# Kernel tuning notes

Measured on AMD Instinct MI355X. Metric: run time of the kernel, lower is better.

The kernel has to match this reference:

```python
import jax, jax.numpy as jnp
import numpy as np

N_ENT, N_REL, RANK = 40943, 11, 256
IMG_DIM, LING_DIM = 1000, 768
BATCH = 1000
ALPHA, GAMMA, SCALE = 0.1, 0.8, 100.0
REG, SINKHORN_ITERS, NUM_OT = 0.05, 100, 10


def _sinkhorn_plan(mm_row, st_row):
    """Entropic-OT plan between uniform marginals over mm_dim and st_dim.
    Cost (as in cal_ot): ((st[:,None]-mm[None,:])**2 * scale).T -> [mm_dim, st_dim].
    Log-domain Sinkhorn for stability. Returns plan of shape [mm_dim, st_dim]."""
    mm_dim, st_dim = mm_row.shape[0], st_row.shape[0]
    M = ((st_row[:, None] - mm_row[None, :]) ** 2 * SCALE).T  # [mm_dim, st_dim]
    logK = -M / REG
    loga = -jnp.log(jnp.float32(mm_dim))  # uniform marginal log-prob
    logb = -jnp.log(jnp.float32(st_dim))
    f0 = jnp.zeros((mm_dim,), M.dtype)
    g0 = jnp.zeros((st_dim,), M.dtype)

    def body(i, fg):
        f, g = fg
        f = REG * (loga - jax.nn.logsumexp(logK + g[None, :] / REG, axis=1))
        g = REG * (logb - jax.nn.logsumexp(logK + f[:, None] / REG, axis=0))
        return (f, g)

    f, g = jax.lax.fori_loop(0, SINKHORN_ITERS, body, (f0, g0))
    return jnp.exp(logK + (f[:, None] + g[None, :]) / REG)


def _cal_ot(mm_vec, st_emb, delta_ot):
    # torch code runs this under no_grad -> stop_gradient on the OT part.
    plans = jax.vmap(_sinkhorn_plan)(mm_vec[:NUM_OT], st_emb[:NUM_OT])  # [10, mm_dim, st_dim]
    st_dim = st_emb.shape[-1]
    return jax.lax.stop_gradient(plans.mean(axis=0) * st_dim * SCALE) + delta_ot


def setup_inputs() -> dict:
    key = jax.random.key(0)
    ks = jax.random.split(key, 9)
    heads = jax.random.randint(ks[0], (BATCH,), 0, N_ENT)
    rels = jax.random.randint(ks[1], (BATCH,), 0, N_REL)
    tails = jax.random.randint(ks[2], (BATCH,), 0, N_ENT)
    x = jnp.stack([heads, rels, tails], axis=1).astype(jnp.int64)
    emb_ent = jax.random.normal(ks[3], (N_ENT, 2 * RANK), jnp.float32) * 0.001
    emb_rel = jax.random.normal(ks[4], (N_REL, 2 * RANK), jnp.float32) * 0.001
    xav_img = float(np.sqrt(2.0 / (IMG_DIM + 2 * RANK)))
    xav_ling = float(np.sqrt(2.0 / (LING_DIM + 2 * RANK)))
    mats_img = jax.random.normal(ks[5], (IMG_DIM, 2 * RANK), jnp.float32) * xav_img
    mats_ling = jax.random.normal(ks[6], (LING_DIM, 2 * RANK), jnp.float32) * xav_ling
    img_vec = jax.random.normal(ks[7], (N_ENT, IMG_DIM), jnp.float32)
    ling_vec = jax.random.normal(ks[8], (N_ENT, LING_DIM), jnp.float32)
    return {"x": x, "emb_ent": emb_ent, "emb_rel": emb_rel, "mats_img": mats_img,
            "mats_ling": mats_ling, "img_vec": img_vec, "ling_vec": ling_vec}


def reference(x, emb_ent, emb_rel, mats_img, mats_ling, img_vec, ling_vec):
    matrix1 = _cal_ot(img_vec, emb_ent, mats_img)    # [img_dim, 2r]
    matrix2 = _cal_ot(ling_vec, emb_ent, mats_ling)  # [ling_dim, 2r]
    img_embeddings = img_vec @ matrix1               # [n_ent, 2r]
    ling_embeddings = ling_vec @ matrix2             # [n_ent, 2r]
    embedding = (1.0 - ALPHA - GAMMA) * emb_ent + ALPHA * img_embeddings + GAMMA * ling_embeddings

    lhs = embedding[x[:, 0]]  # [B, 2r]
    rel = emb_rel[x[:, 1]]
    rhs = embedding[x[:, 2]]
    l0, l1 = lhs[:, :RANK], lhs[:, RANK:]
    r0, r1 = rel[:, :RANK], rel[:, RANK:]
    h0, h1 = rhs[:, :RANK], rhs[:, RANK:]
    t0, t1 = embedding[:, :RANK], embedding[:, RANK:]

    scores = (l0 * r0 - l1 * r1) @ t0.T + (l0 * r1 + l1 * r0) @ t1.T  # [B, n_ent]
    factors = (jnp.sqrt(l0 ** 2 + l1 ** 2),
               jnp.sqrt(r0 ** 2 + r1 ** 2),
               jnp.sqrt(h0 ** 2 + h1 ** 2))
    return scores, factors
```

## Files before the change

kernel.cpp:

```cpp
#include <hip/hip_runtime.h>

#define NENT 40943

typedef short bf16x8 __attribute__((ext_vector_type(8)));
typedef float f32x4 __attribute__((ext_vector_type(4)));

__device__ __forceinline__ unsigned short f2bf(float f) {
  unsigned int u = __builtin_bit_cast(unsigned int, f);
  u += 0x7fffu + ((u >> 16) & 1u);
  return (unsigned short)(u >> 16);
}
__device__ __forceinline__ float bf2f(unsigned short h) {
  unsigned int u = ((unsigned int)h) << 16;
  return __builtin_bit_cast(float, u);
}

#define K2C 2885.3900817779268f

__device__ __forceinline__ float aload(const float* p) {
  return __hip_atomic_load(p, __ATOMIC_RELAXED, __HIP_MEMORY_SCOPE_AGENT);
}
__device__ __forceinline__ void astore(float* p, float v) {
  __hip_atomic_store(p, v, __ATOMIC_RELAXED, __HIP_MEMORY_SCOPE_AGENT);
}

__global__ void init_k(const float* __restrict__ emb_ent, const float* __restrict__ img,
                       const float* __restrict__ ling, float* __restrict__ phi,
                       float* __restrict__ gam, float* __restrict__ A2, float* __restrict__ B2,
                       float* __restrict__ C2, unsigned int* __restrict__ flags) {
  const int p = blockIdx.x, t = threadIdx.x;
  const int pm = p % 10;
  const bool isImg = (p < 10);
  const int D = isImg ? 1000 : 768;
  const float* st = emb_ent + (size_t)pm * 512;
  const float* mm = isImg ? (img + (size_t)pm * 1000) : (ling + (size_t)pm * 768);
  for (int s = t; s < 512; s += 256) {
    float sv = st[s];
    A2[p * 512 + s] = -K2C * sv * sv;
    B2[p * 512 + s] = 2.f * K2C * sv;
    gam[p * 512 + s] = 0.f;
  }
  for (int m = t; m < 1024; m += 256) {
    float c2 = 0.f;
    if (m < D) { float mv = mm[m]; c2 = -K2C * mv * mv; }
    C2[p * 1024 + m] = c2;
    phi[p * 1024 + m] = 0.f;
  }
  if (t < 12) flags[p * 192 + t * 16] = 0u;
}

__global__ __launch_bounds__(512) void sinkhorn_k(
    const float* __restrict__ img, const float* __restrict__ ling,
    float* __restrict__ phi, float* __restrict__ gam,
    const float* __restrict__ A2, const float* __restrict__ B2,
    const float* __restrict__ C2, unsigned int* __restrict__ flags) {
  const int bid = blockIdx.x;
  const int p = bid / 12, j = bid % 12;
  const int pm = p % 10;
  const bool isImg = (p < 10);
  const int D = isImg ? 1000 : 768;
  const float* mm = isImg ? (img + (size_t)pm * 1000) : (ling + (size_t)pm * 768);
  float* phiP = phi + p * 1024;
  float* gamP = gam + p * 512;
  const float* A2P = A2 + p * 512;
  const float* B2P = B2 + p * 512;
  const float* C2P = C2 + p * 1024;
  unsigned int* flagP = flags + p * 192;
  const float negLog2D = isImg ? -9.965784284662087f : -9.584962500721156f;

  const int TPMF = isImg ? 6 : 8;
  const int fChunk = isImg ? 84 : 64;
  const int fm0 = j * fChunk;
  int fCount = D - fm0; if (fCount > fChunk) fCount = fChunk;
  const int gs0 = j * 43;
  int gCount = 512 - gs0; if (gCount > 43) gCount = 43;

  __shared__ float2 wb[512];
  __shared__ float2 um[1024];
  __shared__ float redM[512];
  __shared__ float redA[512];

  const int t = threadIdx.x;
  if (t < 512) wb[t].y = B2P[t];
  for (int m = t; m < D; m += 512) um[m].y = mm[m];

  const int fml = t / TPMF, fq = t - fml * TPMF;
  const bool fAct = (fml < fCount);
  const int fs0 = (fq * 512) / TPMF, fs1 = ((fq + 1) * 512) / TPMF;
  const int fmG = fm0 + fml;
  float fmm = 0.f, fC2 = 0.f;
  if (fAct) { fmm = mm[fmG]; fC2 = C2P[fmG]; }

  const int TPMG = 11;
  const int gsl = t / TPMG, gq = t - gsl * TPMG;
  const bool gAct = (gsl < gCount);
  const int gm0 = (gq * D) / TPMG, gm1 = ((gq + 1) * D) / TPMG;
  const int gsG = gs0 + gsl;
  float gA2 = 0.f;
  if (gAct) gA2 = A2P[gsG];

  unsigned int phase = 0;

  for (int it = 0; it < 100; ++it) {
    if (t < 512) wb[t].x = A2P[t] + aload(&gamP[t]);
    __syncthreads();
    if (fAct) {
      float vmax = -3.0e38f;
      for (int s = fs0; s < fs1; ++s) {
        float2 w = wb[s];
        vmax = fmaxf(vmax, fmaf(w.y, fmm, w.x));
      }
      float acc = 0.f;
      for (int s = fs0; s < fs1; ++s) {
        float2 w = wb[s];
        acc += __builtin_exp2f(fmaf(w.y, fmm, w.x) - vmax);
      }
      redM[t] = vmax; redA[t] = acc;
    }
    __syncthreads();
    if (fAct && fq == 0) {
      float vmax = redM[t], acc = redA[t];
      for (int q = 1; q < TPMF; ++q) {
        float m2 = redM[t + q], a2 = redA[t + q];
        float M = fmaxf(vmax, m2);
        acc = acc * __builtin_exp2f(vmax - M) + a2 * __builtin_exp2f(m2 - M);
        vmax = M;
      }
      astore(&phiP[fmG], negLog2D - fC2 - vmax - __builtin_log2f(acc));
    }
    phase++;
    __syncthreads();
    if (t == 0)
      __hip_atomic_store(flagP + j * 16, phase, __ATOMIC_RELAXED, __HIP_MEMORY_SCOPE_AGENT);
    if (t < 12) {
      while (__hip_atomic_load(flagP + t * 16, __ATOMIC_RELAXED, __HIP_MEMORY_SCOPE_AGENT) < phase)
        __builtin_amdgcn_s_sleep(1);
    }
    __syncthreads();

    for (int m = t; m < D; m += 512) um[m].x = C2P[m] + aload(&phiP[m]);
    __syncthreads();
    if (gAct) {
      float bs = wb[gsG].y;
      float vmax = -3.0e38f;
      for (int m = gm0; m < gm1; ++m) {
        float2 u = um[m];
        vmax = fmaxf(vmax, fmaf(u.y, bs, u.x));
      }
      float acc = 0.f;
      for (int m = gm0; m < gm1; ++m) {
        float2 u = um[m];
        acc += __builtin_exp2f(fmaf(u.y, bs, u.x) - vmax);
      }
      redM[t] = vmax; redA[t] = acc;
    }
    __syncthreads();
    if (gAct && gq == 0) {
      float vmax = redM[t], acc = redA[t];
      for (int q = 1; q < TPMG; ++q) {
        float m2 = redM[t + q], a2 = redA[t + q];
        float M = fmaxf(vmax, m2);
        acc = acc * __builtin_exp2f(vmax - M) + a2 * __builtin_exp2f(m2 - M);
        vmax = M;
      }
      astore(&gamP[gsG], -9.0f - gA2 - vmax - __builtin_log2f(acc));
    }
    phase++;
    __syncthreads();
    if (t == 0)
      __hip_atomic_store(flagP + j * 16, phase, __ATOMIC_RELAXED, __HIP_MEMORY_SCOPE_AGENT);
    if (t < 12) {
      while (__hip_atomic_load(flagP + t * 16, __ATOMIC_RELAXED, __HIP_MEMORY_SCOPE_AGENT) < phase)
        __builtin_amdgcn_s_sleep(1);
    }
    __syncthreads();
  }
}

__global__ void build_b(const float* __restrict__ mats_img, const float* __restrict__ mats_ling,
                        const float* __restrict__ img, const float* __restrict__ ling,
                        const float* __restrict__ phi, const float* __restrict__ gam,
                        const float* __restrict__ A2, const float* __restrict__ B2,
                        const float* __restrict__ C2, unsigned short* __restrict__ BbigT) {
  const int k = blockIdx.x, t = threadIdx.x;
  if (k >= 1768) {
    for (int n = t; n < 512; n += 256) BbigT[(size_t)n * 1792 + k] = 0;
    return;
  }
  const bool isImg = (k < 1000);
  const int kk = isImg ? k : (k - 1000);
  __shared__ float sU[10], sMM[10];
  if (t < 10) {
    const int p = isImg ? t : (10 + t);
    sU[t] = C2[p * 1024 + kk] + phi[p * 1024 + kk];
    sMM[t] = isImg ? img[(size_t)t * 1000 + kk] : ling[(size_t)t * 768 + kk];
  }
  __syncthreads();
  const float* mats = isImg ? mats_img : mats_ling;
  const float scale = isImg ? 0.1f : 0.8f;
  const int pbase = isImg ? 0 : 10;
  for (int n = t; n < 512; n += 256) {
    float val = 0.f;
    #pragma unroll
    for (int i = 0; i < 10; ++i) {
      const int p = pbase + i;
      float a = A2[p * 512 + n] + gam[p * 512 + n];
      float b = B2[p * 512 + n];
      val += __builtin_exp2f(fmaf(b, sMM[i], a + sU[i]));
    }
    float outv = scale * fmaf(5120.f, val, mats[(size_t)kk * 512 + n]);
    BbigT[(size_t)n * 1792 + k] = f2bf(outv);
  }
}

__global__ __launch_bounds__(256) void gemm1_k(
    const float* __restrict__ img, const float* __restrict__ ling,
    const float* __restrict__ emb_ent, const unsigned short* __restrict__ BbigT,
    unsigned short* __restrict__ Eb) {
  const int bid0 = blockIdx.x;
  const int wg = (bid0 & 7) * 160 + (bid0 >> 3);
  const int nt = wg & 3, mt = wg >> 2;
  const int m0 = mt * 128, n0 = nt * 128;
  __shared__ __align__(16) unsigned short As[128 * 40];
  __shared__ __align__(16) unsigned short Bs[128 * 40];
  const int t = threadIdx.x;
  const int wave = t >> 6, lane = t & 63;
  const int quad = lane >> 4, lrow = lane & 15;
  const int wm = (wave & 1) * 64, wn = (wave >> 1) * 64;
  f32x4 acc[4][4];
  #pragma unroll
  for (int a = 0; a < 4; ++a)
    #pragma unroll
    for (int b = 0; b < 4; ++b) acc[a][b] = (f32x4){0.f, 0.f, 0.f, 0.f};

  const int r = t >> 1, h = t & 1;
  const int gm = m0 + r;
  const bool mOK = (gm < NENT);
  const float* arowI = img + (size_t)gm * 1000;
  const float* arowL = ling + (size_t)gm * 768;
  const unsigned short* brow = BbigT + (size_t)(n0 + r) * 1792;
  unsigned short* asDst = As + r * 40 + h * 16;
  unsigned short* bsDst = Bs + r * 40 + h * 16;

  for (int k0 = 0; k0 < 1792; k0 += 32) {
    const int ck = k0 + h * 16;
    unsigned short u[16];
    #pragma unroll
    for (int q4 = 0; q4 < 4; ++q4) {
      const int kk = ck + q4 * 4;
      f32x4 v = (f32x4){0.f, 0.f, 0.f, 0.f};
      if (mOK) {
        if (kk < 1000) v = *(const f32x4*)(arowI + kk);
        else if (kk < 1768) v = *(const f32x4*)(arowL + (kk - 1000));
      }
      u[q4 * 4 + 0] = f2bf(v.x); u[q4 * 4 + 1] = f2bf(v.y);
      u[q4 * 4 + 2] = f2bf(v.z); u[q4 * 4 + 3] = f2bf(v.w);
    }
    bf16x8 w0, w1;
    #pragma unroll
    for (int i2 = 0; i2 < 8; ++i2) { w0[i2] = (short)u[i2]; w1[i2] = (short)u[8 + i2]; }
    *(bf16x8*)asDst = w0;
    *(bf16x8*)(asDst + 8) = w1;
    bf16x8 b0 = *(const bf16x8*)(brow + ck);
    bf16x8 b1 = *(const bf16x8*)(brow + ck + 8);
    *(bf16x8*)bsDst = b0;
    *(bf16x8*)(bsDst + 8) = b1;
    __syncthreads();
    bf16x8 af[4], bfv[4];
    #pragma unroll
    for (int i2 = 0; i2 < 4; ++i2) {
      af[i2] = *(const bf16x8*)(As + (wm + i2 * 16 + lrow) * 40 + quad * 8);
      bfv[i2] = *(const bf16x8*)(Bs + (wn + i2 * 16 + lrow) * 40 + quad * 8);
    }
    #pragma unroll
    for (int mi = 0; mi < 4; ++mi)
      #pragma unroll
      for (int ni = 0; ni < 4; ++ni)
        acc[mi][ni] = __builtin_amdgcn_mfma_f32_16x16x32_bf16(af[mi], bfv[ni], acc[mi][ni], 0, 0, 0);
    __syncthreads();
  }
  #pragma unroll
  for (int mi = 0; mi < 4; ++mi) {
    const int mbase = m0 + wm + mi * 16 + quad * 4;
    #pragma unroll
    for (int ni = 0; ni < 4; ++ni) {
      const int n = n0 + wn + ni * 16 + lrow;
      #pragma unroll
      for (int rr = 0; rr < 4; ++rr) {
        const int gm2 = mbase + rr;
        if (gm2 < NENT) {
          float v = acc[mi][ni][rr] + 0.1f * emb_ent[(size_t)gm2 * 512 + n];
          Eb[(size_t)gm2 * 512 + n] = f2bf(v);
        }
      }
    }
  }
}

__global__ void gather_c(const int* __restrict__ x, const unsigned short* __restrict__ Eb,
                         const float* __restrict__ emb_rel, unsigned short* __restrict__ cb,
                         float* __restrict__ outF) {
  const int i = blockIdx.x, t = threadIdx.x;
  if (i >= 1000) {
    cb[(size_t)i * 512 + t] = 0;
    cb[(size_t)i * 512 + 256 + t] = 0;
    return;
  }
  const int hI = x[i * 3 + 0], rI = x[i * 3 + 1], tI = x[i * 3 + 2];
  const float l0 = bf2f(Eb[(size_t)hI * 512 + t]);
  const float l1 = bf2f(Eb[(size_t)hI * 512 + 256 + t]);
  const float r0 = emb_rel[(size_t)rI * 512 + t];
  const float r1 = emb_rel[(size_t)rI * 512 + 256 + t];
  const float h0 = bf2f(Eb[(size_t)tI * 512 + t]);
  const float h1 = bf2f(Eb[(size_t)tI * 512 + 256 + t]);
  cb[(size_t)i * 512 + t] = f2bf(l0 * r0 - l1 * r1);
  cb[(size_t)i * 512 + 256 + t] = f2bf(l0 * r1 + l1 * r0);
  outF[(size_t)i * 256 + t] = sqrtf(l0 * l0 + l1 * l1);
  outF[256000 + (size_t)i * 256 + t] = sqrtf(r0 * r0 + r1 * r1);
  outF[512000 + (size_t)i * 256 + t] = sqrtf(h0 * h0 + h1 * h1);
}

__global__ __launch_bounds__(256) void gemm2_k(
    const unsigned short* __restrict__ cb, const unsigned short* __restrict__ Eb,
    float* __restrict__ scores) {
  const int bid0 = blockIdx.x;
  const int wg = (bid0 & 7) * 320 + (bid0 >> 3);
  const int mt = wg & 7, nt = wg >> 3;
  const int m0 = mt * 128, n0 = nt * 128;
  __shared__ __align__(16) unsigned short As[128 * 40];
  __shared__ __align__(16) unsigned short Bs[128 * 40];
  const int t = threadIdx.x;
  const int wave = t >> 6, lane = t & 63;
  const int quad = lane >> 4, lrow = lane & 15;
  const int wm = (wave & 1) * 64, wn = (wave >> 1) * 64;
  f32x4 acc[4][4];
  #pragma unroll
  for (int a = 0; a < 4; ++a)
    #pragma unroll
    for (int b = 0; b < 4; ++b) acc[a][b] = (f32x4){0.f, 0.f, 0.f, 0.f};

  const int r = t >> 1, h = t & 1;
  const unsigned short* arow = cb + (size_t)(m0 + r) * 512;
  const int ge = n0 + r;
  const bool nOK = (ge < NENT);
  const unsigned short* browE = Eb + (size_t)ge * 512;
  unsigned short* asDst = As + r * 40 + h * 16;
  unsigned short* bsDst = Bs + r * 40 + h * 16;

  for (int k0 = 0; k0 < 512; k0 += 32) {
    const int ck = k0 + h * 16;
    bf16x8 a0 = *(const bf16x8*)(arow + ck);
    bf16x8 a1 = *(const bf16x8*)(arow + ck + 8);
    *(bf16x8*)asDst = a0;
    *(bf16x8*)(asDst + 8) = a1;
    bf16x8 b0 = (bf16x8)0, b1 = (bf16x8)0;
    if (nOK) { b0 = *(const bf16x8*)(browE + ck); b1 = *(const bf16x8*)(browE + ck + 8); }
    *(bf16x8*)bsDst = b0;
    *(bf16x8*)(bsDst + 8) = b1;
    __syncthreads();
    bf16x8 af[4], bfv[4];
    #pragma unroll
    for (int i2 = 0; i2 < 4; ++i2) {
      af[i2] = *(const bf16x8*)(As + (wm + i2 * 16 + lrow) * 40 + quad * 8);
      bfv[i2] = *(const bf16x8*)(Bs + (wn + i2 * 16 + lrow) * 40 + quad * 8);
    }
    #pragma unroll
    for (int mi = 0; mi < 4; ++mi)
      #pragma unroll
      for (int ni = 0; ni < 4; ++ni)
        acc[mi][ni] = __builtin_amdgcn_mfma_f32_16x16x32_bf16(af[mi], bfv[ni], acc[mi][ni], 0, 0, 0);
    __syncthreads();
  }
  #pragma unroll
  for (int mi = 0; mi < 4; ++mi) {
    const int mbase = m0 + wm + mi * 16 + quad * 4;
    #pragma unroll
    for (int ni = 0; ni < 4; ++ni) {
      const int n = n0 + wn + ni * 16 + lrow;
      if (n < NENT) {
        #pragma unroll
        for (int rr = 0; rr < 4; ++rr) {
          const int i = mbase + rr;
          if (i < 1000) scores[(size_t)i * NENT + n] = acc[mi][ni][rr];
        }
      }
    }
  }
}

extern "C" void kernel_launch(void* const* d_in, const int* in_sizes, int n_in,
                              void* d_out, int out_size, void* d_ws, size_t ws_size,
                              hipStream_t stream) {
  (void)in_sizes; (void)n_in; (void)out_size; (void)ws_size;
  const int*   x        = (const int*)d_in[0];
  const float* emb_ent  = (const float*)d_in[1];
  const float* emb_rel  = (const float*)d_in[2];
  const float* mats_img = (const float*)d_in[3];
  const float* mats_ling= (const float*)d_in[4];
  const float* img_vec  = (const float*)d_in[5];
  const float* ling_vec = (const float*)d_in[6];
  float* out = (float*)d_out;

  float* phi = (float*)d_ws;
  float* gam = phi + 20 * 1024;
  float* A2  = gam + 20 * 512;
  float* B2  = A2 + 20 * 512;
  float* C2  = B2 + 20 * 512;
  unsigned int* flags = (unsigned int*)(C2 + 20 * 1024);
  unsigned short* BbigT = (unsigned short*)(flags + 20 * 192);
  unsigned short* Eb = BbigT + (size_t)512 * 1792;
  unsigned short* cb = Eb + (size_t)NENT * 512;

  init_k<<<dim3(20), dim3(256), 0, stream>>>(emb_ent, img_vec, ling_vec, phi, gam, A2, B2, C2, flags);
  sinkhorn_k<<<dim3(240), dim3(512), 0, stream>>>(img_vec, ling_vec, phi, gam, A2, B2, C2, flags);
  build_b<<<dim3(1792), dim3(256), 0, stream>>>(mats_img, mats_ling, img_vec, ling_vec,
                                                phi, gam, A2, B2, C2, BbigT);
  gemm1_k<<<dim3(1280), dim3(256), 0, stream>>>(img_vec, ling_vec, emb_ent, BbigT, Eb);
  gather_c<<<dim3(1024), dim3(256), 0, stream>>>(x, Eb, emb_rel, cb, out + (size_t)1000 * NENT);
  gemm2_k<<<dim3(2560), dim3(256), 0, stream>>>(cb, Eb, out);
}
```

Baseline: 3.163 ms.

## Replace in-kernel grid barrier Sinkhorn loop with per-iteration kernel launches

After: 3.512 ms. 11.1% more time.

```diff
diff --git a/kernel.cpp b/kernel.cpp
--- a/kernel.cpp
+++ b/kernel.cpp
@@ -17,17 +17,10 @@
 
 #define K2C 2885.3900817779268f
 
-__device__ __forceinline__ float aload(const float* p) {
-  return __hip_atomic_load(p, __ATOMIC_RELAXED, __HIP_MEMORY_SCOPE_AGENT);
-}
-__device__ __forceinline__ void astore(float* p, float v) {
-  __hip_atomic_store(p, v, __ATOMIC_RELAXED, __HIP_MEMORY_SCOPE_AGENT);
-}
-
 __global__ void init_k(const float* __restrict__ emb_ent, const float* __restrict__ img,
                        const float* __restrict__ ling, float* __restrict__ phi,
                        float* __restrict__ gam, float* __restrict__ A2, float* __restrict__ B2,
-                       float* __restrict__ C2, unsigned int* __restrict__ flags) {
+                       float* __restrict__ C2) {
   const int p = blockIdx.x, t = threadIdx.x;
   const int pm = p % 10;
   const bool isImg = (p < 10);
@@ -46,14 +39,13 @@
     C2[p * 1024 + m] = c2;
     phi[p * 1024 + m] = 0.f;
   }
-  if (t < 12) flags[p * 192 + t * 16] = 0u;
-}
-
-__global__ __launch_bounds__(512) void sinkhorn_k(
+}
+
+__global__ __launch_bounds__(512) void sink_f(
     const float* __restrict__ img, const float* __restrict__ ling,
-    float* __restrict__ phi, float* __restrict__ gam,
+    float* __restrict__ phi, const float* __restrict__ gam,
     const float* __restrict__ A2, const float* __restrict__ B2,
-    const float* __restrict__ C2, unsigned int* __restrict__ flags) {
+    const float* __restrict__ C2) {
   const int bid = blockIdx.x;
   const int p = bid / 12, j = bid % 12;
   const int pm = p % 10;
@@ -61,28 +53,24 @@
   const int D = isImg ? 1000 : 768;
   const float* mm = isImg ? (img + (size_t)pm * 1000) : (ling + (size_t)pm * 768);
   float* phiP = phi + p * 1024;
-  float* gamP = gam + p * 512;
+  const float* gamP = gam + p * 512;
   const float* A2P = A2 + p * 512;
   const float* B2P = B2 + p * 512;
   const float* C2P = C2 + p * 1024;
-  unsigned int* flagP = flags + p * 192;
   const float negLog2D = isImg ? -9.965784284662087f : -9.584962500721156f;
 
   const int TPMF = isImg ? 6 : 8;
   const int fChunk = isImg ? 84 : 64;
   const int fm0 = j * fChunk;
   int fCount = D - fm0; if (fCount > fChunk) fCount = fChunk;
-  const int gs0 = j * 43;
-  int gCount = 512 - gs0; if (gCount > 43) gCount = 43;
 
   __shared__ float2 wb[512];
-  __shared__ float2 um[1024];
   __shared__ float redM[512];
   __shared__ float redA[512];
 
   const int t = threadIdx.x;
-  if (t < 512) wb[t].y = B2P[t];
-  for (int m = t; m < D; m += 512) um[m].y = mm[m];
+  wb[t].x = A2P[t] + gamP[t];
+  wb[t].y = B2P[t];
 
   const int fml = t / TPMF, fq = t - fml * TPMF;
   const bool fAct = (fml < fCount);
@@ -90,90 +78,96 @@
   const int fmG = fm0 + fml;
   float fmm = 0.f, fC2 = 0.f;
   if (fAct) { fmm = mm[fmG]; fC2 = C2P[fmG]; }
+  __syncthreads();
+
+  if (fAct) {
+    float vmax = -3.0e38f;
+    for (int s = fs0; s < fs1; ++s) {
+      float2 w = wb[s];
+      vmax = fmaxf(vmax, fmaf(w.y, fmm, w.x));
+    }
+    float acc = 0.f;
+    for (int s = fs0; s < fs1; ++s) {
+      float2 w = wb[s];
+      acc += __builtin_exp2f(fmaf(w.y, fmm, w.x) - vmax);
+    }
+    redM[t] = vmax; redA[t] = acc;
+  }
+  __syncthreads();
+  if (fAct && fq == 0) {
+    float vmax = redM[t], acc = redA[t];
+    for (int q = 1; q < TPMF; ++q) {
+      float m2 = redM[t + q], a2 = redA[t + q];
+      float M = fmaxf(vmax, m2);
+      acc = acc * __builtin_exp2f(vmax - M) + a2 * __builtin_exp2f(m2 - M);
+      vmax = M;
+    }
+    phiP[fmG] = negLog2D - fC2 - vmax - __builtin_log2f(acc);
+  }
+}
+
+__global__ __launch_bounds__(512) void sink_g(
+    const float* __restrict__ img, const float* __restrict__ ling,
+    const float* __restrict__ phi, float* __restrict__ gam,
+    const float* __restrict__ A2, const float* __restrict__ B2,
+    const float* __restrict__ C2) {
+  const int bid = blockIdx.x;
+  const int p = bid / 12, j = bid % 12;
+  const int pm = p % 10;
+  const bool isImg = (p < 10);
+  const int D = isImg ? 1000 : 768;
+  const float* mm = isImg ? (img + (size_t)pm * 1000) : (ling + (size_t)pm * 768);
+  const float* phiP = phi + p * 1024;
+  float* gamP = gam + p * 512;
+  const float* A2P = A2 + p * 512;
+  const float* B2P = B2 + p * 512;
+  const float* C2P = C2 + p * 1024;
+
+  const int gs0 = j * 43;
+  int gCount = 512 - gs0; if (gCount > 43) gCount = 43;
+
+  __shared__ float2 um[1024];
+  __shared__ float redM[512];
+  __shared__ float redA[512];
+
+  const int t = threadIdx.x;
+  for (int m = t; m < D; m += 512) {
+    um[m].x = C2P[m] + phiP[m];
+    um[m].y = mm[m];
+  }
 
   const int TPMG = 11;
   const int gsl = t / TPMG, gq = t - gsl * TPMG;
   const bool gAct = (gsl < gCount);
   const int gm0 = (gq * D) / TPMG, gm1 = ((gq + 1) * D) / TPMG;
   const int gsG = gs0 + gsl;
-  float gA2 = 0.f;
-  if (gAct) gA2 = A2P[gsG];
-
-  unsigned int phase = 0;
-
-  for (int it = 0; it < 100; ++it) {
-    if (t < 512) wb[t].x = A2P[t] + aload(&gamP[t]);
-    __syncthreads();
-    if (fAct) {
-      float vmax = -3.0e38f;
-      for (int s = fs0; s < fs1; ++s) {
-        float2 w = wb[s];
-        vmax = fmaxf(vmax, fmaf(w.y, fmm, w.x));
-      }
-      float acc = 0.f;
-      for (int s = fs0; s < fs1; ++s) {
-        float2 w = wb[s];
-        acc += __builtin_exp2f(fmaf(w.y, fmm, w.x) - vmax);
-      }
-      redM[t] = vmax; redA[t] = acc;
-    }
-    __syncthreads();
-    if (fAct && fq == 0) {
-      float vmax = redM[t], acc = redA[t];
-      for (int q = 1; q < TPMF; ++q) {
-        float m2 = redM[t + q], a2 = redA[t + q];
-        float M = fmaxf(vmax, m2);
-        acc = acc * __builtin_exp2f(vmax - M) + a2 * __builtin_exp2f(m2 - M);
-        vmax = M;
-      }
-      astore(&phiP[fmG], negLog2D - fC2 - vmax - __builtin_log2f(acc));
-    }
-    phase++;
-    __syncthreads();
-    if (t == 0)
-      __hip_atomic_store(flagP + j * 16, phase, __ATOMIC_RELAXED, __HIP_MEMORY_SCOPE_AGENT);
-    if (t < 12) {
-      while (__hip_atomic_load(flagP + t * 16, __ATOMIC_RELAXED, __HIP_MEMORY_SCOPE_AGENT) < phase)
-        __builtin_amdgcn_s_sleep(1);
-    }
-    __syncthreads();
-
-    for (int m = t; m < D; m += 512) um[m].x = C2P[m] + aload(&phiP[m]);
-    __syncthreads();
-    if (gAct) {
-      float bs = wb[gsG].y;
-      float vmax = -3.0e38f;
-      for (int m = gm0; m < gm1; ++m) {
-        float2 u = um[m];
-        vmax = fmaxf(vmax, fmaf(u.y, bs, u.x));
-      }
-      float acc = 0.f;
-      for (int m = gm0; m < gm1; ++m) {
-        float2 u = um[m];
-        acc += __builtin_exp2f(fmaf(u.y, bs, u.x) - vmax);
-      }
-      redM[t] = vmax; redA[t] = acc;
-    }
-    __syncthreads();
-    if (gAct && gq == 0) {
-      float vmax = redM[t], acc = redA[t];
-      for (int q = 1; q < TPMG; ++q) {
-        float m2 = redM[t + q], a2 = redA[t + q];
-        float M = fmaxf(vmax, m2);
-        acc = acc * __builtin_exp2f(vmax - M) + a2 * __builtin_exp2f(m2 - M);
-        vmax = M;
-      }
-      astore(&gamP[gsG], -9.0f - gA2 - vmax - __builtin_log2f(acc));
-    }
-    phase++;
-    __syncthreads();
-    if (t == 0)
-      __hip_atomic_store(flagP + j * 16, phase, __ATOMIC_RELAXED, __HIP_MEMORY_SCOPE_AGENT);
-    if (t < 12) {
-      while (__hip_atomic_load(flagP + t * 16, __ATOMIC_RELAXED, __HIP_MEMORY_SCOPE_AGENT) < phase)
-        __builtin_amdgcn_s_sleep(1);
-    }
-    __syncthreads();
+  float gA2 = 0.f, bs = 0.f;
+  if (gAct) { gA2 = A2P[gsG]; bs = B2P[gsG]; }
+  __syncthreads();
+
+  if (gAct) {
+    float vmax = -3.0e38f;
+    for (int m = gm0; m < gm1; ++m) {
+      float2 u = um[m];
+      vmax = fmaxf(vmax, fmaf(u.y, bs, u.x));
+    }
+    float acc = 0.f;
+    for (int m = gm0; m < gm1; ++m) {
+      float2 u = um[m];
+      acc += __builtin_exp2f(fmaf(u.y, bs, u.x) - vmax);
+    }
+    redM[t] = vmax; redA[t] = acc;
+  }
+  __syncthreads();
+  if (gAct && gq == 0) {
+    float vmax = redM[t], acc = redA[t];
+    for (int q = 1; q < TPMG; ++q) {
+      float m2 = redM[t + q], a2 = redA[t + q];
+      float M = fmaxf(vmax, m2);
+      acc = acc * __builtin_exp2f(vmax - M) + a2 * __builtin_exp2f(m2 - M);
+      vmax = M;
+    }
+    gamP[gsG] = -9.0f - gA2 - vmax - __builtin_log2f(acc);
   }
 }
 
@@ -406,13 +400,15 @@
   float* A2  = gam + 20 * 512;
   float* B2  = A2 + 20 * 512;
   float* C2  = B2 + 20 * 512;
-  unsigned int* flags = (unsigned int*)(C2 + 20 * 1024);
-  unsigned short* BbigT = (unsigned short*)(flags + 20 * 192);
+  unsigned short* BbigT = (unsigned short*)(C2 + 20 * 1024);
   unsigned short* Eb = BbigT + (size_t)512 * 1792;
   unsigned short* cb = Eb + (size_t)NENT * 512;
 
-  init_k<<<dim3(20), dim3(256), 0, stream>>>(emb_ent, img_vec, ling_vec, phi, gam, A2, B2, C2, flags);
-  sinkhorn_k<<<dim3(240), dim3(512), 0, stream>>>(img_vec, ling_vec, phi, gam, A2, B2, C2, flags);
+  init_k<<<dim3(20), dim3(256), 0, stream>>>(emb_ent, img_vec, ling_vec, phi, gam, A2, B2, C2);
+  for (int it = 0; it < 100; ++it) {
+    sink_f<<<dim3(240), dim3(512), 0, stream>>>(img_vec, ling_vec, phi, gam, A2, B2, C2);
+    sink_g<<<dim3(240), dim3(512), 0, stream>>>(img_vec, ling_vec, phi, gam, A2, B2, C2);
+  }
   build_b<<<dim3(1792), dim3(256), 0, stream>>>(mats_img, mats_ling, img_vec, ling_vec,
                                                 phi, gam, A2, B2, C2, BbigT);
   gemm1_k<<<dim3(1280), dim3(256), 0, stream>>>(img_vec, ling_vec, emb_ent, BbigT, Eb);
```

## Replace per-phase flag barriers with tagged per-element values in Sinkhorn

Applied to the files above, without the earlier changes.

Result: no change. 3.163 ms (+0.0%).

```diff
diff --git a/kernel.cpp b/kernel.cpp
--- a/kernel.cpp
+++ b/kernel.cpp
@@ -4,6 +4,7 @@
 
 typedef short bf16x8 __attribute__((ext_vector_type(8)));
 typedef float f32x4 __attribute__((ext_vector_type(4)));
+typedef unsigned long long u64;
 
 __device__ __forceinline__ unsigned short f2bf(float f) {
   unsigned int u = __builtin_bit_cast(unsigned int, f);
@@ -17,17 +18,27 @@
 
 #define K2C 2885.3900817779268f
 
-__device__ __forceinline__ float aload(const float* p) {
-  return __hip_atomic_load(p, __ATOMIC_RELAXED, __HIP_MEMORY_SCOPE_AGENT);
-}
-__device__ __forceinline__ void astore(float* p, float v) {
+__device__ __forceinline__ float tval(u64 v) {
+  return __builtin_bit_cast(float, (unsigned int)(v & 0xffffffffu));
+}
+__device__ __forceinline__ float tagged_poll(const u64* p, unsigned int tag) {
+  u64 v;
+  for (;;) {
+    v = __hip_atomic_load(p, __ATOMIC_RELAXED, __HIP_MEMORY_SCOPE_AGENT);
+    if ((unsigned int)(v >> 32) >= tag) break;
+    __builtin_amdgcn_s_sleep(1);
+  }
+  return tval(v);
+}
+__device__ __forceinline__ void tagged_store(u64* p, unsigned int tag, float f) {
+  u64 v = ((u64)tag << 32) | (u64)__builtin_bit_cast(unsigned int, f);
   __hip_atomic_store(p, v, __ATOMIC_RELAXED, __HIP_MEMORY_SCOPE_AGENT);
 }
 
 __global__ void init_k(const float* __restrict__ emb_ent, const float* __restrict__ img,
-                       const float* __restrict__ ling, float* __restrict__ phi,
-                       float* __restrict__ gam, float* __restrict__ A2, float* __restrict__ B2,
-                       float* __restrict__ C2, unsigned int* __restrict__ flags) {
+                       const float* __restrict__ ling, u64* __restrict__ phiT,
+                       u64* __restrict__ gamT, float* __restrict__ A2, float* __restrict__ B2,
+                       float* __restrict__ C2) {
   const int p = blockIdx.x, t = threadIdx.x;
   const int pm = p % 10;
   const bool isImg = (p < 10);
@@ -38,34 +49,32 @@
     float sv = st[s];
     A2[p * 512 + s] = -K2C * sv * sv;
     B2[p * 512 + s] = 2.f * K2C * sv;
-    gam[p * 512 + s] = 0.f;
+    gamT[p * 512 + s] = 0ull;
   }
   for (int m = t; m < 1024; m += 256) {
     float c2 = 0.f;
     if (m < D) { float mv = mm[m]; c2 = -K2C * mv * mv; }
     C2[p * 1024 + m] = c2;
-    phi[p * 1024 + m] = 0.f;
-  }
-  if (t < 12) flags[p * 192 + t * 16] = 0u;
+    phiT[p * 1024 + m] = 0ull;
+  }
 }
 
 __global__ __launch_bounds__(512) void sinkhorn_k(
     const float* __restrict__ img, const float* __restrict__ ling,
-    float* __restrict__ phi, float* __restrict__ gam,
+    u64* __restrict__ phiT, u64* __restrict__ gamT,
     const float* __restrict__ A2, const float* __restrict__ B2,
-    const float* __restrict__ C2, unsigned int* __restrict__ flags) {
+    const float* __restrict__ C2) {
   const int bid = blockIdx.x;
   const int p = bid / 12, j = bid % 12;
   const int pm = p % 10;
   const bool isImg = (p < 10);
   const int D = isImg ? 1000 : 768;
   const float* mm = isImg ? (img + (size_t)pm * 1000) : (ling + (size_t)pm * 768);
-  float* phiP = phi + p * 1024;
-  float* gamP = gam + p * 512;
+  u64* phiP = phiT + p * 1024;
+  u64* gamP = gamT + p * 512;
   const float* A2P = A2 + p * 512;
   const float* B2P = B2 + p * 512;
   const float* C2P = C2 + p * 1024;
-  unsigned int* flagP = flags + p * 192;
   const float negLog2D = isImg ? -9.965784284662087f : -9.584962500721156f;
 
   const int TPMF = isImg ? 6 : 8;
@@ -81,8 +90,9 @@
   __shared__ float redA[512];
 
   const int t = threadIdx.x;
-  if (t < 512) wb[t].y = B2P[t];
+  wb[t].y = B2P[t];
   for (int m = t; m < D; m += 512) um[m].y = mm[m];
+  const float wbA2 = A2P[t];
 
   const int fml = t / TPMF, fq = t - fml * TPMF;
   const bool fAct = (fml < fCount);
@@ -99,10 +109,11 @@
   float gA2 = 0.f;
   if (gAct) gA2 = A2P[gsG];
 
-  unsigned int phase = 0;
-
   for (int it = 0; it < 100; ++it) {
-    if (t < 512) wb[t].x = A2P[t] + aload(&gamP[t]);
+    const unsigned int gtag = 2u * (unsigned)it;
+    const unsigned int ptag = 2u * (unsigned)it + 1u;
+
+    wb[t].x = wbA2 + tagged_poll(&gamP[t], gtag);
     __syncthreads();
     if (fAct) {
       float vmax = -3.0e38f;
@@ -126,19 +137,10 @@
         acc = acc * __builtin_exp2f(vmax - M) + a2 * __builtin_exp2f(m2 - M);
         vmax = M;
       }
-      astore(&phiP[fmG], negLog2D - fC2 - vmax - __builtin_log2f(acc));
-    }
-    phase++;
-    __syncthreads();
-    if (t == 0)
-      __hip_atomic_store(flagP + j * 16, phase, __ATOMIC_RELAXED, __HIP_MEMORY_SCOPE_AGENT);
-    if (t < 12) {
-      while (__hip_atomic_load(flagP + t * 16, __ATOMIC_RELAXED, __HIP_MEMORY_SCOPE_AGENT) < phase)
-        __builtin_amdgcn_s_sleep(1);
-    }
-    __syncthreads();
-
-    for (int m = t; m < D; m += 512) um[m].x = C2P[m] + aload(&phiP[m]);
+      tagged_store(&phiP[fmG], ptag, negLog2D - fC2 - vmax - __builtin_log2f(acc));
+    }
+
+    for (int m = t; m < D; m += 512) um[m].x = C2P[m] + tagged_poll(&phiP[m], ptag);
     __syncthreads();
     if (gAct) {
       float bs = wb[gsG].y;
@@ -163,15 +165,7 @@
         acc = acc * __builtin_exp2f(vmax - M) + a2 * __builtin_exp2f(m2 - M);
         vmax = M;
       }
-      astore(&gamP[gsG], -9.0f - gA2 - vmax - __builtin_log2f(acc));
-    }
-    phase++;
-    __syncthreads();
-    if (t == 0)
-      __hip_atomic_store(flagP + j * 16, phase, __ATOMIC_RELAXED, __HIP_MEMORY_SCOPE_AGENT);
-    if (t < 12) {
-      while (__hip_atomic_load(flagP + t * 16, __ATOMIC_RELAXED, __HIP_MEMORY_SCOPE_AGENT) < phase)
-        __builtin_amdgcn_s_sleep(1);
+      tagged_store(&gamP[gsG], gtag + 2u, -9.0f - gA2 - vmax - __builtin_log2f(acc));
     }
     __syncthreads();
   }
@@ -179,7 +173,7 @@
 
 __global__ void build_b(const float* __restrict__ mats_img, const float* __restrict__ mats_ling,
                         const float* __restrict__ img, const float* __restrict__ ling,
-                        const float* __restrict__ phi, const float* __restrict__ gam,
+                        const u64* __restrict__ phiT, const u64* __restrict__ gamT,
                         const float* __restrict__ A2, const float* __restrict__ B2,
                         const float* __restrict__ C2, unsigned short* __restrict__ BbigT) {
   const int k = blockIdx.x, t = threadIdx.x;
@@ -192,7 +186,7 @@
   __shared__ float sU[10], sMM[10];
   if (t < 10) {
     const int p = isImg ? t : (10 + t);
-    sU[t] = C2[p * 1024 + kk] + phi[p * 1024 + kk];
+    sU[t] = C2[p * 1024 + kk] + tval(phiT[p * 1024 + kk]);
     sMM[t] = isImg ? img[(size_t)t * 1000 + kk] : ling[(size_t)t * 768 + kk];
   }
   __syncthreads();
@@ -204,7 +198,7 @@
     #pragma unroll
     for (int i = 0; i < 10; ++i) {
       const int p = pbase + i;
-      float a = A2[p * 512 + n] + gam[p * 512 + n];
+      float a = A2[p * 512 + n] + tval(gamT[p * 512 + n]);
       float b = B2[p * 512 + n];
       val += __builtin_exp2f(fmaf(b, sMM[i], a + sU[i]));
     }
@@ -401,20 +395,19 @@
   const float* ling_vec = (const float*)d_in[6];
   float* out = (float*)d_out;
 
-  float* phi = (float*)d_ws;
-  float* gam = phi + 20 * 1024;
-  float* A2  = gam + 20 * 512;
+  u64* phiT = (u64*)d_ws;
+  u64* gamT = phiT + 20 * 1024;
+  float* A2  = (float*)(gamT + 20 * 512);
   float* B2  = A2 + 20 * 512;
   float* C2  = B2 + 20 * 512;
-  unsigned int* flags = (unsigned int*)(C2 + 20 * 1024);
-  unsigned short* BbigT = (unsigned short*)(flags + 20 * 192);
+  unsigned short* BbigT = (unsigned short*)(C2 + 20 * 1024);
   unsigned short* Eb = BbigT + (size_t)512 * 1792;
   unsigned short* cb = Eb + (size_t)NENT * 512;
 
-  init_k<<<dim3(20), dim3(256), 0, stream>>>(emb_ent, img_vec, ling_vec, phi, gam, A2, B2, C2, flags);
-  sinkhorn_k<<<dim3(240), dim3(512), 0, stream>>>(img_vec, ling_vec, phi, gam, A2, B2, C2, flags);
+  init_k<<<dim3(20), dim3(256), 0, stream>>>(emb_ent, img_vec, ling_vec, phiT, gamT, A2, B2, C2);
+  sinkhorn_k<<<dim3(240), dim3(512), 0, stream>>>(img_vec, ling_vec, phiT, gamT, A2, B2, C2);
   build_b<<<dim3(1792), dim3(256), 0, stream>>>(mats_img, mats_ling, img_vec, ling_vec,
-                                                phi, gam, A2, B2, C2, BbigT);
+                                                phiT, gamT, A2, B2, C2, BbigT);
   gemm1_k<<<dim3(1280), dim3(256), 0, stream>>>(img_vec, ling_vec, emb_ent, BbigT, Eb);
   gather_c<<<dim3(1024), dim3(256), 0, stream>>>(x, Eb, emb_rel, cb, out + (size_t)1000 * NENT);
   gemm2_k<<<dim3(2560), dim3(256), 0, stream>>>(cb, Eb, out);
```
